# Optimization experiments

Hardware: AMD Instinct MI355X
Metric: run time of the kernel (lower is better)

The kernel has to match this reference:

```python
import jax, jax.numpy as jnp
import numpy as np

N_HASHES = 4
N_BUCKETS = 8
NUM_HEADS = 8
LN_EPS = 1e-5


def layer_norm(x, g, b):
    m = jnp.mean(x, axis=-1, keepdims=True)
    v = jnp.mean(jnp.square(x - m), axis=-1, keepdims=True)
    return (x - m) * jax.lax.rsqrt(v + LN_EPS) * g + b


def setup_inputs() -> dict:
    key = jax.random.key(0)
    ks = jax.random.split(key, 8)
    B, N, C = 16, 8192, 256
    dff = 4 * C
    w = 0.05  # weight init scale
    return {
        'x': jax.random.normal(ks[0], (B, N, C), jnp.float32),
        'rotations': jax.random.normal(ks[1], (1, C, N_HASHES, N_BUCKETS // 2), jnp.float32),
        'norm1_g': jnp.ones((C,), jnp.float32),
        'norm1_b': jnp.zeros((C,), jnp.float32),
        'q_w': jax.random.normal(ks[2], (C, C), jnp.float32) * w,
        'kv_w': jax.random.normal(ks[3], (C, 2 * C), jnp.float32) * w,
        'norm2_g': jnp.ones((C,), jnp.float32),
        'norm2_b': jnp.zeros((C,), jnp.float32),
        'fc1_w': jax.random.normal(ks[4], (C, dff), jnp.float32) * w,
        'fc1_b': jnp.zeros((dff,), jnp.float32),
        'fc2_w': jax.random.normal(ks[5], (dff, C), jnp.float32) * w,
        'fc2_b': jnp.zeros((C,), jnp.float32),
    }


def reference(x, rotations, norm1_g, norm1_b, q_w, kv_w, norm2_g, norm2_b, fc1_w, fc1_b, fc2_w, fc2_b):
    B, N, C = x.shape
    H = NUM_HEADS
    Dh = C // H
    scale = Dh ** -0.5

    x_ = layer_norm(x, norm1_g, norm1_b)

    # q: [B, H, N, Dh]
    q = (x_ @ q_w).reshape(B, N, H, Dh).transpose(0, 2, 1, 3)

    # --- hash_vectors: LSH bucket assignment + scatter-pool ---
    # rotated: [B, n_hashes, N, n_buckets//2] -> concat with negation -> n_buckets
    rotated = jnp.einsum('btf,fhi->bhti', x_, rotations[0])
    rotated = jnp.concatenate([rotated, -rotated], axis=-1)
    buckets = jnp.argmax(rotated, axis=-1)                      # [B, n_hashes, N]
    one_hot = jax.nn.one_hot(buckets, N_BUCKETS, dtype=x.dtype)  # [B, n_hashes, N, n_buckets]
    sum_buckets = jnp.sum(one_hot, axis=2)                       # [B, n_hashes, n_buckets]
    pooled = jnp.einsum('bnf,bhni->bhif', x_, one_hot)           # [B, n_hashes, n_buckets, C]
    pooled = pooled / (jax.lax.stop_gradient(sum_buckets)[..., None] + 1e-20)
    rp_x = pooled.reshape(B, N_HASHES * N_BUCKETS, C)            # [B, M, C] pooled KV tokens
    sumb = jax.lax.stop_gradient(sum_buckets.reshape(B, N_HASHES * N_BUCKETS))

    # kv: [2, B, H, M, Dh]
    M = N_HASHES * N_BUCKETS
    kv = (rp_x @ kv_w).reshape(B, M, 2, H, Dh).transpose(2, 0, 3, 1, 4)
    k, v = kv[0], kv[1]

    # masked attention over pooled buckets
    attn = jnp.einsum('bhnd,bhmd->bhnm', q, k) * scale           # [B, H, N, M]
    mask = (sumb >= 1)[:, None, None, :]                          # [B, 1, 1, M]
    attn = jnp.where(mask, attn, -jnp.finfo(attn.dtype).max)
    attn = jax.nn.softmax(attn, axis=-1)
    out = jnp.einsum('bhnm,bhmd->bnhd', attn, v).reshape(B, N, C)
    x = x + out

    # MLP block (GELU is exact erf, matching torch nn.GELU default)
    y = layer_norm(x, norm2_g, norm2_b)
    h = jax.nn.gelu(y @ fc1_w + fc1_b, approximate=False)
    y = h @ fc2_w + fc2_b
    return x + y
```

## Files before the change

kernel.cpp:

```cpp
#include <hip/hip_runtime.h>
#include <hip/hip_bf16.h>
#include <float.h>
#include <math.h>

#define Bn   16
#define Nn   8192
#define Cn   256
#define Hn   8
#define DHn  32
#define Mn   32
#define DFFn 1024
#define TOK  64

typedef __attribute__((ext_vector_type(8))) short short8;
typedef __attribute__((ext_vector_type(4))) float f32x4;

typedef const __attribute__((address_space(1))) unsigned int* gas_t;
typedef __attribute__((address_space(3))) unsigned int* las_t;

__device__ __forceinline__ float bf2f(ushort u) {
    union { unsigned int i; float f; } v; v.i = ((unsigned int)u) << 16; return v.f;
}
__device__ __forceinline__ ushort f2bf(float f) {
    union { float f; unsigned int i; } v; v.f = f;
    unsigned int r = (v.i + 0x7fffu + ((v.i >> 16) & 1u)) >> 16;
    return (ushort)r;
}

__device__ __forceinline__ float gelu_erf(float v) {
    const float z  = v * 0.70710678118654752f;
    const float az = fabsf(z);
    const float t  = __builtin_amdgcn_rcpf(1.f + 0.3275911f * az);
    float poly = t * (0.254829592f + t * (-0.284496736f +
                 t * (1.421413741f + t * (-1.453152027f + t * 1.061405429f))));
    const float e    = __expf(-az * az);
    const float erfa = 1.f - poly * e;
    const float erfz = copysignf(erfa, z);
    return 0.5f * v * (1.f + erfz);
}

__global__ __launch_bounds__(256, 4) void ln1_pool_kernel(
    const float* __restrict__ x, const float* __restrict__ rot,
    const float* __restrict__ g1, const float* __restrict__ b1,
    ushort* __restrict__ xbf, float* __restrict__ pool_part, float* __restrict__ cnt_part)
{
    __shared__ ushort xt[TOK][Cn];
    __shared__ unsigned int idsS[TOK];

    const int tid  = threadIdx.x;
    const int w    = tid >> 6, lane = tid & 63;
    const int o    = lane & 15;
    const int g    = lane >> 4;
    const int fbase = g << 6;

    float rwv[64];
    #pragma unroll
    for (int f = 0; f < 64; ++f) rwv[f] = rot[(fbase + f) * 16 + o];

    const int b  = blockIdx.x >> 7;
    const int n0 = (blockIdx.x & 127) << 6;

    const float4 gv = *(const float4*)&g1[lane * 4];
    const float4 bv = *(const float4*)&b1[lane * 4];

    for (int it = 0; it < TOK / 4; ++it) {
        const int tloc = (it << 2) + w;
        const size_t roff = ((size_t)b * Nn + n0 + tloc) * Cn;
        float4 xv = *(const float4*)&x[roff + lane * 4];
        float s  = xv.x + xv.y + xv.z + xv.w;
        float s2 = xv.x * xv.x + xv.y * xv.y + xv.z * xv.z + xv.w * xv.w;
        #pragma unroll
        for (int msk = 1; msk < 64; msk <<= 1) { s += __shfl_xor(s, msk); s2 += __shfl_xor(s2, msk); }
        float mean = s * (1.f / Cn);
        float var  = s2 * (1.f / Cn) - mean * mean;
        float rr   = rsqrtf(var + 1e-5f);
        float xn[4];
        xn[0] = (xv.x - mean) * rr * gv.x + bv.x;
        xn[1] = (xv.y - mean) * rr * gv.y + bv.y;
        xn[2] = (xv.z - mean) * rr * gv.z + bv.z;
        xn[3] = (xv.w - mean) * rr * gv.w + bv.w;
        ushort4 ub; ub.x = f2bf(xn[0]); ub.y = f2bf(xn[1]); ub.z = f2bf(xn[2]); ub.w = f2bf(xn[3]);
        *(ushort4*)&xbf[roff + lane * 4] = ub;
        *(ushort4*)&xt[tloc][lane * 4] = ub;

        float d = 0.f;
        #pragma unroll
        for (int j = 0; j < 8; ++j) {
            short8 xs = *(const short8*)&xt[tloc][fbase + j * 8];
            #pragma unroll
            for (int u = 0; u < 8; ++u)
                d += bf2f((ushort)xs[u]) * rwv[j * 8 + u];
        }
        d += __shfl_xor(d, 16); d += __shfl_xor(d, 32);

        float d0 = __shfl(d, (lane & 12));
        float d1 = __shfl(d, (lane & 12) | 1);
        float d2 = __shfl(d, (lane & 12) | 2);
        float d3 = __shfl(d, (lane & 12) | 3);
        int bk = 0; float bb = d0;
        if (d1  > bb) { bb = d1;  bk = 1; }
        if (d2  > bb) { bb = d2;  bk = 2; }
        if (d3  > bb) { bb = d3;  bk = 3; }
        if (-d0 > bb) { bb = -d0; bk = 4; }
        if (-d1 > bb) { bb = -d1; bk = 5; }
        if (-d2 > bb) { bb = -d2; bk = 6; }
        if (-d3 > bb) { bb = -d3; bk = 7; }
        const unsigned int bk0 = __shfl(bk, 0), bk1 = __shfl(bk, 4),
                           bk2 = __shfl(bk, 8), bk3 = __shfl(bk, 12);
        if (lane == 0)
            idsS[tloc] = bk0 | (bk1 << 8) | (bk2 << 16) | (bk3 << 24);
    }
    __syncthreads();

    float pool[Mn];
    #pragma unroll
    for (int m = 0; m < Mn; ++m) pool[m] = 0.f;
    for (int t = 0; t < TOK; ++t) {
        const float xv = bf2f(xt[t][tid]);
        const unsigned int idw = idsS[t];
        #pragma unroll
        for (int h = 0; h < 4; ++h) {
            const unsigned int id = (idw >> (8 * h)) & 7u;
            #pragma unroll
            for (int mb = 0; mb < 8; ++mb)
                pool[h * 8 + mb] += (id == (unsigned int)mb) ? xv : 0.f;
        }
    }
    const size_t pbase = (size_t)blockIdx.x * (Mn * Cn);
    #pragma unroll
    for (int m = 0; m < Mn; ++m)
        pool_part[pbase + m * Cn + tid] = pool[m];

    if (tid < Mn) {
        const int h = tid >> 3, mb = tid & 7;
        float c = 0.f;
        for (int t = 0; t < TOK; ++t)
            c += (((idsS[t] >> (8 * h)) & 255u) == (unsigned int)mb) ? 1.f : 0.f;
        cnt_part[blockIdx.x * Mn + tid] = c;
    }
}

__global__ __launch_bounds__(256) void kv_kernel(
    const float* __restrict__ pool_part, const float* __restrict__ cnt_part,
    const float* __restrict__ kv_w, float* __restrict__ kbuf, float* __restrict__ vbuf,
    float* __restrict__ countsF)
{
    __shared__ float rp[Cn];
    const int tid = threadIdx.x;
    const int b = blockIdx.x >> 5;
    const int m = blockIdx.x & 31;

    float acc = 0.f, cnt = 0.f;
    for (int j = 0; j < 128; ++j) {
        const int blk = b * 128 + j;
        acc += pool_part[(size_t)blk * (Mn * Cn) + m * Cn + tid];
        cnt += cnt_part[blk * Mn + m];
    }
    rp[tid] = acc / (cnt + 1e-20f);
    if (tid == 0) countsF[b * Mn + m] = cnt;
    __syncthreads();

    float a0 = 0.f, a1 = 0.f;
    for (int f = 0; f < Cn; ++f) {
        float rv = rp[f];
        a0 += rv * kv_w[f * 512 + tid];
        a1 += rv * kv_w[f * 512 + 256 + tid];
    }
    const int h = tid >> 5, d = tid & 31;
    kbuf[(((size_t)b * Hn + h) * Mn + m) * DHn + d] = a0;
    vbuf[(((size_t)b * Hn + h) * Mn + m) * DHn + d] = a1;
}

__global__ __launch_bounds__(256) void ws_build_kernel(
    const float* __restrict__ q_w, const float* __restrict__ kbuf, ushort* __restrict__ WsT)
{
    __shared__ float kSh[Mn * DHn];
    const int tid = threadIdx.x;
    const int b = blockIdx.x >> 3, h = blockIdx.x & 7;
    for (int i = tid; i < Mn * DHn; i += 256)
        kSh[i] = kbuf[((size_t)(b * Hn + h) * Mn) * DHn + i];
    __syncthreads();

    float qr[32];
    #pragma unroll
    for (int i = 0; i < 8; ++i) {
        float4 v = *(const float4*)&q_w[(size_t)tid * Cn + h * DHn + i * 4];
        qr[i*4+0] = v.x; qr[i*4+1] = v.y; qr[i*4+2] = v.z; qr[i*4+3] = v.w;
    }
    #pragma unroll 4
    for (int m = 0; m < Mn; ++m) {
        float s = 0.f;
        #pragma unroll
        for (int d = 0; d < DHn; ++d) s += qr[d] * kSh[m * DHn + d];
        WsT[((size_t)b * Cn + h * Mn + m) * Cn + tid] = f2bf(s * 0.17677669529663687f);
    }
}

template<int EPI>
__global__ __launch_bounds__(256) void gemm_bt(
    const ushort* __restrict__ A, const ushort* __restrict__ Bt,
    const float* __restrict__ bias, const float* __restrict__ resid,
    void* __restrict__ Cp, int Mrows, int Ncols, int K, int bstride)
{
    __shared__ ushort As[128 * 32];
    __shared__ ushort Bs[128 * 32];
    const int tid  = threadIdx.x;
    const int lane = tid & 63;
    const int w    = tid >> 6;
    const int wm   = (w >> 1) << 6;
    const int wn   = (w & 1) << 6;
    const int lr   = lane & 15;
    const int lq   = lane >> 4;
    const int m0   = blockIdx.y << 7;
    const int n0   = blockIdx.x << 7;
    const ushort* Btb = Bt + (size_t)(m0 >> 13) * (size_t)bstride;

    const int srcRow = lane >> 2;
    const int srcCol = (lane & 3) << 3;
    const ushort* gA0 = &A  [(size_t)(m0 + w * 16      + srcRow) * K + srcCol];
    const ushort* gA1 = &A  [(size_t)(m0 + (w + 4) * 16 + srcRow) * K + srcCol];
    const ushort* gB0 = &Btb[(size_t)(n0 + w * 16      + srcRow) * K + srcCol];
    const ushort* gB1 = &Btb[(size_t)(n0 + (w + 4) * 16 + srcRow) * K + srcCol];
    ushort* lA0 = &As[ w      * 512];
    ushort* lA1 = &As[(w + 4) * 512];
    ushort* lB0 = &Bs[ w      * 512];
    ushort* lB1 = &Bs[(w + 4) * 512];

    f32x4 acc[4][4];
    #pragma unroll
    for (int i = 0; i < 4; i++)
        #pragma unroll
        for (int j = 0; j < 4; j++)
            acc[i][j] = (f32x4){0.f, 0.f, 0.f, 0.f};

    for (int k0 = 0; k0 < K; k0 += 32) {
        __builtin_amdgcn_global_load_lds((gas_t)(const void*)(gA0 + k0), (las_t)(void*)lA0, 16, 0, 0);
        __builtin_amdgcn_global_load_lds((gas_t)(const void*)(gA1 + k0), (las_t)(void*)lA1, 16, 0, 0);
        __builtin_amdgcn_global_load_lds((gas_t)(const void*)(gB0 + k0), (las_t)(void*)lB0, 16, 0, 0);
        __builtin_amdgcn_global_load_lds((gas_t)(const void*)(gB1 + k0), (las_t)(void*)lB1, 16, 0, 0);
        __syncthreads();
        short8 af[4], bfr[4];
        #pragma unroll
        for (int i = 0; i < 4; i++) af[i]  = *(const short8*)&As[(wm + i * 16 + lr) * 32 + lq * 8];
        #pragma unroll
        for (int j = 0; j < 4; j++) bfr[j] = *(const short8*)&Bs[(wn + j * 16 + lr) * 32 + lq * 8];
        #pragma unroll
        for (int i = 0; i < 4; i++)
            #pragma unroll
            for (int j = 0; j < 4; j++)
                acc[i][j] = __builtin_amdgcn_mfma_f32_16x16x32_bf16(af[i], bfr[j], acc[i][j], 0, 0, 0);
        __syncthreads();
    }

    #pragma unroll
    for (int i = 0; i < 4; i++) {
        #pragma unroll
        for (int j = 0; j < 4; j++) {
            const int col = n0 + wn + j * 16 + lr;
            #pragma unroll
            for (int r = 0; r < 4; r++) {
                const int rw = m0 + wm + i * 16 + lq * 4 + r;
                float v = acc[i][j][r];
                if (EPI == 1) { v += bias[col]; v = gelu_erf(v); }
                if (EPI == 2) {
                    v += bias[col] + resid[(size_t)rw * Ncols + col];
                    ((float*)Cp)[(size_t)rw * Ncols + col] = v;
                } else {
                    ((ushort*)Cp)[(size_t)rw * Ncols + col] = f2bf(v);
                }
            }
        }
    }
}

#define VS3 1028
#define OB3 260

__global__ __launch_bounds__(256) void attn3_ln2_kernel(
    const ushort* __restrict__ S, const float* __restrict__ vbuf,
    const float* __restrict__ counts, const float* __restrict__ x,
    const float* __restrict__ g2, const float* __restrict__ b2,
    float* __restrict__ x2, ushort* __restrict__ ybf)
{
    __shared__ float vS[Hn * VS3];
    __shared__ float outb[32 * OB3];
    __shared__ float mS[32], rS[32];
    __shared__ unsigned int mkS;

    const int tid = threadIdx.x;
    const int b = blockIdx.x >> 8;
    const int nbase = (blockIdx.x & 255) << 5;

    for (int i = tid; i < Hn * Mn * DHn; i += 256)
        vS[(i >> 10) * VS3 + (i & 1023)] = vbuf[(size_t)b * (Hn * Mn * DHn) + i];
    {
        float cv = (tid < Mn) ? counts[b * Mn + tid] : 0.f;
        unsigned long long bal = __ballot(tid < Mn && cv >= 1.f);
        if (tid == 0) mkS = (unsigned int)bal;
    }
    __syncthreads();
    const unsigned int mk = mkS;

    const int t = tid >> 3;
    const int h = tid & 7;
    const int n = nbase + t;
    const size_t off = ((size_t)b * Nn + n) * Cn + h * DHn;

    float p[32];
    #pragma unroll
    for (int u = 0; u < 4; ++u) {
        short8 sv = *(const short8*)&S[off + u * 8];
        #pragma unroll
        for (int j = 0; j < 8; ++j) p[u * 8 + j] = bf2f((ushort)sv[j]);
    }
    float mx = -FLT_MAX;
    #pragma unroll
    for (int m = 0; m < 32; ++m) {
        if (!((mk >> m) & 1u)) p[m] = -FLT_MAX;
        mx = fmaxf(mx, p[m]);
    }
    float den = 0.f;
    #pragma unroll
    for (int m = 0; m < 32; ++m) { p[m] = __expf(p[m] - mx); den += p[m]; }
    const float inv = 1.f / den;

    float o[32];
    #pragma unroll
    for (int i = 0; i < 32; ++i) o[i] = 0.f;
    const float* vbase = &vS[h * VS3];
    #pragma unroll
    for (int m = 0; m < 32; ++m) {
        const float pm = p[m];
        const float* vp = vbase + m * DHn;
        #pragma unroll
        for (int dq = 0; dq < 8; ++dq) {
            float4 v4 = *(const float4*)&vp[dq * 4];
            o[dq*4+0] += pm * v4.x; o[dq*4+1] += pm * v4.y;
            o[dq*4+2] += pm * v4.z; o[dq*4+3] += pm * v4.w;
        }
    }

    float s = 0.f, s2 = 0.f;
    #pragma unroll
    for (int dq = 0; dq < 8; ++dq) {
        float4 xv = *(const float4*)&x[off + dq * 4];
        float r0 = xv.x + o[dq*4+0] * inv;
        float r1 = xv.y + o[dq*4+1] * inv;
        float r2 = xv.z + o[dq*4+2] * inv;
        float r3 = xv.w + o[dq*4+3] * inv;
        *(float4*)&outb[t * OB3 + h * DHn + dq * 4] = make_float4(r0, r1, r2, r3);
        s  += r0 + r1 + r2 + r3;
        s2 += r0*r0 + r1*r1 + r2*r2 + r3*r3;
    }
    #pragma unroll
    for (int msk = 1; msk < 8; msk <<= 1) {
        s += __shfl_xor(s, msk); s2 += __shfl_xor(s2, msk);
    }
    if (h == 0) {
        const float mean = s * (1.f / Cn);
        const float var  = s2 * (1.f / Cn) - mean * mean;
        mS[t] = mean;
        rS[t] = rsqrtf(var + 1e-5f);
    }
    __syncthreads();

    const int lane = tid & 63;
    const float4 g4 = *(const float4*)&g2[lane * 4];
    const float4 b4 = *(const float4*)&b2[lane * 4];
    const size_t gbase = ((size_t)b * Nn + nbase) * Cn;
    #pragma unroll
    for (int j = 0; j < 8; ++j) {
        const int e   = j * 1024 + tid * 4;
        const int row = e >> 8;
        const int c   = e & 255;
        float4 rv = *(const float4*)&outb[row * OB3 + c];
        *(float4*)&x2[gbase + e] = rv;
        const float mean = mS[row], rr = rS[row];
        ushort4 yb;
        yb.x = f2bf((rv.x - mean) * rr * g4.x + b4.x);
        yb.y = f2bf((rv.y - mean) * rr * g4.y + b4.y);
        yb.z = f2bf((rv.z - mean) * rr * g4.z + b4.z);
        yb.w = f2bf((rv.w - mean) * rr * g4.w + b4.w);
        *(ushort4*)&ybf[gbase + e] = yb;
    }
}

__global__ void wcast_kernel(const float* __restrict__ W, ushort* __restrict__ Wt, int R, int Cc)
{
    int idx = blockIdx.x * 256 + threadIdx.x;
    if (idx < R * Cc) {
        int r = idx / Cc, c = idx % Cc;
        Wt[(size_t)c * R + r] = f2bf(W[idx]);
    }
}

extern "C" void kernel_launch(void* const* d_in, const int* in_sizes, int n_in,
                              void* d_out, int out_size, void* d_ws, size_t ws_size,
                              hipStream_t stream)
{
    const float* x    = (const float*)d_in[0];
    const float* rot  = (const float*)d_in[1];
    const float* n1g  = (const float*)d_in[2];
    const float* n1b  = (const float*)d_in[3];
    const float* q_w  = (const float*)d_in[4];
    const float* kv_w = (const float*)d_in[5];
    const float* n2g  = (const float*)d_in[6];
    const float* n2b  = (const float*)d_in[7];
    const float* fc1w = (const float*)d_in[8];
    const float* fc1b = (const float*)d_in[9];
    const float* fc2w = (const float*)d_in[10];
    const float* fc2b = (const float*)d_in[11];

    char* ws = (char*)d_ws;
    const size_t XBF_OFF = 0;
    const size_t S_OFF   = 67108864ull;
    const size_t H_OFF   = 0;
    const size_t X2_OFF  = 268435456ull;
    const size_t PP_OFF  = X2_OFF;
    const size_t CP_OFF  = X2_OFF + 67108864;
    const size_t Y_OFF   = 402653184ull;
    const size_t CT_OFF  = 469762048ull;
    const size_t KB_OFF  = CT_OFF + 4096;
    const size_t VB_OFF  = KB_OFF + 524288;
    const size_t F1T_OFF = VB_OFF + 524288;
    const size_t F2T_OFF = F1T_OFF + 524288;

    ushort* xbf    = (ushort*)(ws + XBF_OFF);
    ushort* Sbuf   = (ushort*)(ws + S_OFF);
    ushort* hbf    = (ushort*)(ws + H_OFF);
    float*  x2     = (float*)(ws + X2_OFF);
    float*  ppart  = (float*)(ws + PP_OFF);
    float*  cpart  = (float*)(ws + CP_OFF);
    ushort* WsT    = (ushort*)(ws + X2_OFF);
    ushort* ybf    = (ushort*)(ws + Y_OFF);
    float*  countsF= (float*)(ws + CT_OFF);
    float*  kbuf   = (float*)(ws + KB_OFF);
    float*  vbuf   = (float*)(ws + VB_OFF);
    ushort* f1T    = (ushort*)(ws + F1T_OFF);
    ushort* f2T    = (ushort*)(ws + F2T_OFF);

    wcast_kernel<<<dim3(1024), 256, 0, stream>>>(fc1w, f1T, 256, 1024);
    wcast_kernel<<<dim3(1024), 256, 0, stream>>>(fc2w, f2T, 1024, 256);

    ln1_pool_kernel<<<dim3(Bn * 128), 256, 0, stream>>>(x, rot, n1g, n1b, xbf, ppart, cpart);
    kv_kernel<<<dim3(Bn * Mn), 256, 0, stream>>>(ppart, cpart, kv_w, kbuf, vbuf, countsF);
    ws_build_kernel<<<dim3(Bn * Hn), 256, 0, stream>>>(q_w, kbuf, WsT);
    gemm_bt<0><<<dim3(2, 1024), 256, 0, stream>>>(xbf, WsT, nullptr, nullptr, Sbuf, Bn * Nn, Cn, Cn, Cn * Cn);
    attn3_ln2_kernel<<<dim3(Bn * 256), 256, 0, stream>>>(Sbuf, vbuf, countsF, x, n2g, n2b, x2, ybf);
    gemm_bt<1><<<dim3(8, 1024), 256, 0, stream>>>(ybf, f1T, fc1b, nullptr, hbf, Bn * Nn, DFFn, Cn, 0);
    gemm_bt<2><<<dim3(2, 1024), 256, 0, stream>>>(hbf, f2T, fc2b, x2, d_out, Bn * Nn, Cn, DFFn, 0);
}
```

Before: 910.9 us.

## Double-buffer GEMM LDS tiles and remap blocks with XCD-aware swizzle

The bf16 MFMA GEMM now keeps two LDS buffers for A and B. The next K-slice is loaded asynchronously while the current one is computed, which removes one barrier per iteration and overlaps global loads with MFMA work. The launch grid is also flattened to 1D, and block ids are remapped so that consecutive ids spread across the 8 XCDs while neighbouring tiles share L2. This doubles LDS use per block, which may lower occupancy.

```diff
diff --git a/kernel.cpp b/kernel.cpp
--- a/kernel.cpp
+++ b/kernel.cpp
@@ -202,8 +202,8 @@
     const float* __restrict__ bias, const float* __restrict__ resid,
     void* __restrict__ Cp, int Mrows, int Ncols, int K, int bstride)
 {
-    __shared__ ushort As[128 * 32];
-    __shared__ ushort Bs[128 * 32];
+    __shared__ ushort As[2][128 * 32];
+    __shared__ ushort Bs[2][128 * 32];
     const int tid  = threadIdx.x;
     const int lane = tid & 63;
     const int w    = tid >> 6;
@@ -211,20 +211,23 @@
     const int wn   = (w & 1) << 6;
     const int lr   = lane & 15;
     const int lq   = lane >> 4;
-    const int m0   = blockIdx.y << 7;
-    const int n0   = blockIdx.x << 7;
+
+    const int id  = blockIdx.x;
+    const int cpx = gridDim.x >> 3;
+    const int wg  = (id & 7) * cpx + (id >> 3);
+    const int ntx = Ncols >> 7;
+    const int nts = __builtin_ctz(ntx);
+    const int m0  = (wg >> nts) << 7;
+    const int n0  = (wg & (ntx - 1)) << 7;
+
     const ushort* Btb = Bt + (size_t)(m0 >> 13) * (size_t)bstride;
 
     const int srcRow = lane >> 2;
     const int srcCol = (lane & 3) << 3;
-    const ushort* gA0 = &A  [(size_t)(m0 + w * 16      + srcRow) * K + srcCol];
+    const ushort* gA0 = &A  [(size_t)(m0 + w * 16       + srcRow) * K + srcCol];
     const ushort* gA1 = &A  [(size_t)(m0 + (w + 4) * 16 + srcRow) * K + srcCol];
-    const ushort* gB0 = &Btb[(size_t)(n0 + w * 16      + srcRow) * K + srcCol];
+    const ushort* gB0 = &Btb[(size_t)(n0 + w * 16       + srcRow) * K + srcCol];
     const ushort* gB1 = &Btb[(size_t)(n0 + (w + 4) * 16 + srcRow) * K + srcCol];
-    ushort* lA0 = &As[ w      * 512];
-    ushort* lA1 = &As[(w + 4) * 512];
-    ushort* lB0 = &Bs[ w      * 512];
-    ushort* lB1 = &Bs[(w + 4) * 512];
 
     f32x4 acc[4][4];
     #pragma unroll
@@ -233,23 +236,46 @@
         for (int j = 0; j < 4; j++)
             acc[i][j] = (f32x4){0.f, 0.f, 0.f, 0.f};
 
-    for (int k0 = 0; k0 < K; k0 += 32) {
-        __builtin_amdgcn_global_load_lds((gas_t)(const void*)(gA0 + k0), (las_t)(void*)lA0, 16, 0, 0);
-        __builtin_amdgcn_global_load_lds((gas_t)(const void*)(gA1 + k0), (las_t)(void*)lA1, 16, 0, 0);
-        __builtin_amdgcn_global_load_lds((gas_t)(const void*)(gB0 + k0), (las_t)(void*)lB0, 16, 0, 0);
-        __builtin_amdgcn_global_load_lds((gas_t)(const void*)(gB1 + k0), (las_t)(void*)lB1, 16, 0, 0);
-        __syncthreads();
+    const int nt = K >> 5;
+
+    __builtin_amdgcn_global_load_lds((gas_t)(const void*)gA0, (las_t)(void*)&As[0][ w      * 512], 16, 0, 0);
+    __builtin_amdgcn_global_load_lds((gas_t)(const void*)gA1, (las_t)(void*)&As[0][(w + 4) * 512], 16, 0, 0);
+    __builtin_amdgcn_global_load_lds((gas_t)(const void*)gB0, (las_t)(void*)&Bs[0][ w      * 512], 16, 0, 0);
+    __builtin_amdgcn_global_load_lds((gas_t)(const void*)gB1, (las_t)(void*)&Bs[0][(w + 4) * 512], 16, 0, 0);
+    __syncthreads();
+
+    int cur = 0;
+    for (int t = 0; t < nt - 1; ++t) {
+        const int k1 = (t + 1) << 5;
+        const int nxt = cur ^ 1;
+        __builtin_amdgcn_global_load_lds((gas_t)(const void*)(gA0 + k1), (las_t)(void*)&As[nxt][ w      * 512], 16, 0, 0);
+        __builtin_amdgcn_global_load_lds((gas_t)(const void*)(gA1 + k1), (las_t)(void*)&As[nxt][(w + 4) * 512], 16, 0, 0);
+        __builtin_amdgcn_global_load_lds((gas_t)(const void*)(gB0 + k1), (las_t)(void*)&Bs[nxt][ w      * 512], 16, 0, 0);
+        __builtin_amdgcn_global_load_lds((gas_t)(const void*)(gB1 + k1), (las_t)(void*)&Bs[nxt][(w + 4) * 512], 16, 0, 0);
         short8 af[4], bfr[4];
         #pragma unroll
-        for (int i = 0; i < 4; i++) af[i]  = *(const short8*)&As[(wm + i * 16 + lr) * 32 + lq * 8];
-        #pragma unroll
-        for (int j = 0; j < 4; j++) bfr[j] = *(const short8*)&Bs[(wn + j * 16 + lr) * 32 + lq * 8];
+        for (int i = 0; i < 4; i++) af[i]  = *(const short8*)&As[cur][(wm + i * 16 + lr) * 32 + lq * 8];
+        #pragma unroll
+        for (int j = 0; j < 4; j++) bfr[j] = *(const short8*)&Bs[cur][(wn + j * 16 + lr) * 32 + lq * 8];
         #pragma unroll
         for (int i = 0; i < 4; i++)
             #pragma unroll
             for (int j = 0; j < 4; j++)
                 acc[i][j] = __builtin_amdgcn_mfma_f32_16x16x32_bf16(af[i], bfr[j], acc[i][j], 0, 0, 0);
         __syncthreads();
+        cur = nxt;
+    }
+    {
+        short8 af[4], bfr[4];
+        #pragma unroll
+        for (int i = 0; i < 4; i++) af[i]  = *(const short8*)&As[cur][(wm + i * 16 + lr) * 32 + lq * 8];
+        #pragma unroll
+        for (int j = 0; j < 4; j++) bfr[j] = *(const short8*)&Bs[cur][(wn + j * 16 + lr) * 32 + lq * 8];
+        #pragma unroll
+        for (int i = 0; i < 4; i++)
+            #pragma unroll
+            for (int j = 0; j < 4; j++)
+                acc[i][j] = __builtin_amdgcn_mfma_f32_16x16x32_bf16(af[i], bfr[j], acc[i][j], 0, 0, 0);
     }
 
     #pragma unroll
@@ -445,8 +471,8 @@
     ln1_pool_kernel<<<dim3(Bn * 128), 256, 0, stream>>>(x, rot, n1g, n1b, xbf, ppart, cpart);
     kv_kernel<<<dim3(Bn * Mn), 256, 0, stream>>>(ppart, cpart, kv_w, kbuf, vbuf, countsF);
     ws_build_kernel<<<dim3(Bn * Hn), 256, 0, stream>>>(q_w, kbuf, WsT);
-    gemm_bt<0><<<dim3(2, 1024), 256, 0, stream>>>(xbf, WsT, nullptr, nullptr, Sbuf, Bn * Nn, Cn, Cn, Cn * Cn);
+    gemm_bt<0><<<dim3(2 * 1024), 256, 0, stream>>>(xbf, WsT, nullptr, nullptr, Sbuf, Bn * Nn, Cn, Cn, Cn * Cn);
     attn3_ln2_kernel<<<dim3(Bn * 256), 256, 0, stream>>>(Sbuf, vbuf, countsF, x, n2g, n2b, x2, ybf);
-    gemm_bt<1><<<dim3(8, 1024), 256, 0, stream>>>(ybf, f1T, fc1b, nullptr, hbf, Bn * Nn, DFFn, Cn, 0);
-    gemm_bt<2><<<dim3(2, 1024), 256, 0, stream>>>(hbf, f2T, fc2b, x2, d_out, Bn * Nn, Cn, DFFn, 0);
-}
+    gemm_bt<1><<<dim3(8 * 1024), 256, 0, stream>>>(ybf, f1T, fc1b, nullptr, hbf, Bn * Nn, DFFn, Cn, 0);
+    gemm_bt<2><<<dim3(2 * 1024), 256, 0, stream>>>(hbf, f2T, fc2b, x2, d_out, Bn * Nn, Cn, DFFn, 0);
+}
```

New measurement: 877.1 us. 1.04x faster.
